# Kernel optimization log

Measured on AMD Instinct MI355X. Metric: run time of the kernel, lower is better.

The kernel has to match this reference:

```python
import jax, jax.numpy as jnp
import numpy as np

HEADS = 16
DIM = 1024


def setup_inputs() -> dict:
    key = jax.random.key(0)
    ks = jax.random.split(key, 9)
    b, n, d = 2, 2048, DIM
    scale = 1.0 / np.sqrt(d)  # xavier-ish scale for weights
    x = jax.random.normal(ks[0], (b, n, d), dtype=jnp.float32)
    Wq = jax.random.normal(ks[1], (d, d), dtype=jnp.float32) * scale
    Wk = jax.random.normal(ks[2], (d, d), dtype=jnp.float32) * scale
    Wv = jax.random.normal(ks[3], (d, d), dtype=jnp.float32) * scale
    Wo = jax.random.normal(ks[4], (d, d), dtype=jnp.float32) * scale
    bq = jnp.zeros((d,), jnp.float32)
    bk = jnp.zeros((d,), jnp.float32)
    bv = jnp.zeros((d,), jnp.float32)
    bo = jnp.zeros((d,), jnp.float32)
    return {"x": x, "Wq": Wq, "bq": bq, "Wk": Wk, "bk": bk,
            "Wv": Wv, "bv": bv, "Wo": Wo, "bo": bo}


def reference(x, Wq, bq, Wk, bk, Wv, bv, Wo, bo):
    b, n, d = x.shape
    h = HEADS
    hd = d // h
    # torch Linear: y = x @ W.T + b  (W stored [out, in]; here square so W given as [d,d])
    q = x @ Wq.T + bq
    k = x @ Wk.T + bk
    v = x @ Wv.T + bv
    # b n (h d) -> b h n d
    q = q.reshape(b, n, h, hd).transpose(0, 2, 1, 3)
    k = k.reshape(b, n, h, hd).transpose(0, 2, 1, 3)
    v = v.reshape(b, n, h, hd).transpose(0, 2, 1, 3)
    # NOTE: scale is 1/sqrt(dim), not 1/sqrt(head_dim), faithful to source.
    scores = jnp.einsum('bhqd,bhkd->bhqk', q, k) / jnp.sqrt(jnp.float32(d))
    attn = jax.nn.softmax(scores, axis=-1)
    out = jnp.einsum('bhqk,bhkd->bhqd', attn, v)
    out = out.transpose(0, 2, 1, 3).reshape(b, n, d)  # b h n d -> b n (h d)
    return out @ Wo.T + bo
```

## Files before the change

### kernel.cpp

```cpp
#include <hip/hip_runtime.h>

typedef unsigned short u16t;
typedef __attribute__((ext_vector_type(8))) short bf16x8;
typedef __attribute__((ext_vector_type(4))) float f32x4;

#define DM   1024
#define SEQL 2048
#define NHD  16
#define HDD  64

#define GLL16(g, l) __builtin_amdgcn_global_load_lds( \
    (const __attribute__((address_space(1))) void*)(g), \
    (__attribute__((address_space(3))) void*)(l), 16, 0, 0)

#if defined(__has_builtin)
#if __has_builtin(__builtin_amdgcn_exp2f)
#define EXP2(x) __builtin_amdgcn_exp2f(x)
#else
#define EXP2(x) exp2f(x)
#endif
#else
#define EXP2(x) exp2f(x)
#endif

__device__ __forceinline__ u16t f2bf(float f) {
  unsigned u = __float_as_uint(f);
  return (u16t)((u + 0x7fffu + ((u >> 16) & 1u)) >> 16);
}
__device__ __forceinline__ unsigned pack_bf16_2(float a, float b) {
  const unsigned ua = __float_as_uint(a) + 0x8000u;
  const unsigned ub = __float_as_uint(b) + 0x8000u;
  return __builtin_amdgcn_perm(ub, ua, 0x07060302);
}

struct ConvArgs { const float* src[5]; u16t* dst[5]; };

__global__ __launch_bounds__(256) void conv_kernel(ConvArgs a) {
  const int gid = blockIdx.x * 256 + threadIdx.x;
  const int e = gid << 2;
  int sel, off;
  if (e < 4194304) { sel = 0; off = e; }
  else { const int r = e - 4194304; sel = 1 + (r >> 20); off = r & 1048575; }
  const float4 f = *(const float4*)(a.src[sel] + off);
  union { u16t s[4]; uint2 u; } o;
  o.s[0] = f2bf(f.x); o.s[1] = f2bf(f.y); o.s[2] = f2bf(f.z); o.s[3] = f2bf(f.w);
  *(uint2*)(a.dst[sel] + off) = o.u;
}

__device__ __forceinline__ int gslot(int m, int kc) { return (m << 2) + (kc ^ ((m >> 1) & 3)); }

template<int MODE>
__device__ __forceinline__ void qkv_body(
    const u16t* __restrict__ X, const u16t* __restrict__ W,
    const float* __restrict__ bias, float oscale, u16t* __restrict__ outB,
    u16t* smem)
{
  u16t* const Es = smem;

  const int tid = threadIdx.x;
  const int l = tid & 63, w = tid >> 6, q = l >> 4, ln = l & 15;
  const int trow0 = blockIdx.y << 7;
  const int dcol0 = blockIdx.x << 7;
  const int wm = (w >> 1) << 6, wn = (w & 1) << 6;

  const int s0 = (w << 6) + l, s1 = s0 + 256;
  const int m0 = s0 >> 2, kc0 = (s0 & 3) ^ ((m0 >> 1) & 3);
  const int m1 = s1 >> 2, kc1 = (s1 & 3) ^ ((m1 >> 1) & 3);
  const u16t* gA0 = X + (size_t)(trow0 + m0) * DM + (kc0 << 3);
  const u16t* gA1 = X + (size_t)(trow0 + m1) * DM + (kc1 << 3);
  const u16t* gB0 = W + (size_t)(dcol0 + m0) * DM + (kc0 << 3);
  const u16t* gB1 = W + (size_t)(dcol0 + m1) * DM + (kc1 << 3);
  const int dO0 = (w << 6) << 3;
  const int dO1 = ((w << 6) + 256) << 3;

  f32x4 acc[4][4] = {};

  GLL16(gA0, smem + dO0);
  GLL16(gA1, smem + dO1);
  GLL16(gB0, smem + 4096 + dO0);
  GLL16(gB1, smem + 4096 + dO1);

  for (int kt = 0; kt < DM; kt += 32) {
    const int it = kt >> 5;
    u16t* const curA = smem + ((it & 1) ? 8192 : 0);
    u16t* const curB = curA + 4096;
    __syncthreads();
    if (kt + 32 < DM) {
      u16t* const nA = smem + ((it & 1) ? 0 : 8192);
      u16t* const nB = nA + 4096;
      GLL16(gA0 + kt + 32, nA + dO0);
      GLL16(gA1 + kt + 32, nA + dO1);
      GLL16(gB0 + kt + 32, nB + dO0);
      GLL16(gB1 + kt + 32, nB + dO1);
    }

    bf16x8 af[4], bfr[4];
    #pragma unroll
    for (int mi = 0; mi < 4; ++mi) {
      const int r = wm + (mi << 4) + ln;
      af[mi] = *(const bf16x8*)&((MODE == 1 ? curB : curA)[gslot(r, q) << 3]);
    }
    #pragma unroll
    for (int ni = 0; ni < 4; ++ni) {
      const int r = wn + (ni << 4) + ln;
      bfr[ni] = *(const bf16x8*)&((MODE == 1 ? curA : curB)[gslot(r, q) << 3]);
    }
    #pragma unroll
    for (int mi = 0; mi < 4; ++mi)
      #pragma unroll
      for (int ni = 0; ni < 4; ++ni)
        acc[mi][ni] = __builtin_amdgcn_mfma_f32_16x16x32_bf16(af[mi], bfr[ni], acc[mi][ni], 0, 0, 0);
  }

  __syncthreads();

  if (MODE == 1) {
    #pragma unroll
    for (int mi = 0; mi < 4; ++mi) {
      const int dl = wm + (mi << 4) + (q << 2);
      const float4 b4 = *(const float4*)&bias[dcol0 + dl];
      #pragma unroll
      for (int ni = 0; ni < 4; ++ni) {
        const int tl = wn + (ni << 4) + ln;
        uint2 pk;
        pk.x = pack_bf16_2((acc[mi][ni][0] + b4.x) * oscale, (acc[mi][ni][1] + b4.y) * oscale);
        pk.y = pack_bf16_2((acc[mi][ni][2] + b4.z) * oscale, (acc[mi][ni][3] + b4.w) * oscale);
        *(uint2*)&Es[tl * 136 + dl] = pk;
      }
    }
    __syncthreads();
    #pragma unroll
    for (int it = 0; it < 8; ++it) {
      const int u = (it << 8) + tid;
      const int tl = u >> 4, c8 = u & 15;
      const uint4 vv = *(const uint4*)&Es[tl * 136 + (c8 << 3)];
      const int tok = trow0 + tl;
      const int b = tok >> 11, n = tok & (SEQL - 1);
      const int dg = dcol0 + (c8 << 3);
      const int h = dg >> 6, hd = dg & 63;
      *(uint4*)&outB[((size_t)(b * NHD + h) * SEQL + n) * HDD + hd] = vv;
    }
  } else {
    #pragma unroll
    for (int ni = 0; ni < 4; ++ni) {
      const int dl = wn + (ni << 4) + ln;
      const float bv = bias[dcol0 + dl];
      #pragma unroll
      for (int mi = 0; mi < 4; ++mi) {
        const int g = (wm >> 2) + (mi << 2) + q;
        const int g6 = g & 15;
        const int gp = (g & 16) | (g6 & 8) | ((g6 & 3) << 1) | ((g6 >> 2) & 1);
        uint2 pk;
        pk.x = pack_bf16_2(acc[mi][ni][0] + bv, acc[mi][ni][1] + bv);
        pk.y = pack_bf16_2(acc[mi][ni][2] + bv, acc[mi][ni][3] + bv);
        *(uint2*)&Es[dl * 136 + (gp << 2)] = pk;
      }
    }
    __syncthreads();
    #pragma unroll
    for (int it = 0; it < 8; ++it) {
      const int u = (it << 8) + tid;
      const int dl = u >> 4, c8 = u & 15;
      const uint4 vv = *(const uint4*)&Es[dl * 136 + (c8 << 3)];
      const int dg = dcol0 + dl;
      const int h = dg >> 6, hd = dg & 63;
      const int b = trow0 >> 11;
      const int n = (trow0 & (SEQL - 1)) + (c8 << 3);
      *(uint4*)&outB[((size_t)(b * NHD + h) * HDD + hd) * SEQL + n] = vv;
    }
  }
}

struct QKVArgs { const u16t* W[3]; const float* b[3]; u16t* dst[3]; };

__global__ __launch_bounds__(256) void qkv_kernel(const u16t* __restrict__ X, QKVArgs g) {
  __shared__ alignas(16) u16t smem[17408];
  const int z = blockIdx.z;
  if (z == 2)      qkv_body<2>(X, g.W[2], g.b[2], 1.0f, g.dst[2], smem);
  else if (z == 1) qkv_body<1>(X, g.W[1], g.b[1], 1.0f, g.dst[1], smem);
  else             qkv_body<1>(X, g.W[0], g.b[0], 0.04508422f, g.dst[0], smem);
}

__global__ __launch_bounds__(256, 4) void attn_kernel(
    const u16t* __restrict__ Qb, const u16t* __restrict__ Kb,
    const u16t* __restrict__ Vt, u16t* __restrict__ ctx)
{
  __shared__ alignas(16) u16t smem[16384];

  const int tid = threadIdx.x;
  const int l = tid & 63, w = tid >> 6;
  const int q = l >> 4, ln = l & 15;
  const int bh = blockIdx.x, q0 = blockIdx.y << 7;
  const size_t hb = (size_t)bh * SEQL * HDD;
  const u16t* Qg = Qb + hb;
  const u16t* Kg = Kb + hb;
  const u16t* Vg = Vt + hb;

  bf16x8 qf[2][2];
  #pragma unroll
  for (int g = 0; g < 2; ++g) {
    const int qr = q0 + (w << 5) + (g << 4) + ln;
    #pragma unroll
    for (int ks = 0; ks < 2; ++ks)
      qf[g][ks] = *(const bf16x8*)(Qg + (size_t)qr * HDD + (((ks << 2) + q) << 3));
  }

  const int u0 = tid,       r0 = u0 >> 3, c0 = (u0 & 7) ^ (r0 & 7);
  const int u1 = 256 + tid, r1 = u1 >> 3, c1 = (u1 & 7) ^ (r1 & 7);
  const u16t* const kS0 = Kg + (size_t)r0 * HDD + (c0 << 3);
  const u16t* const kS1 = Kg + (size_t)r1 * HDD + (c1 << 3);
  const u16t* const vS0 = Vg + (size_t)r0 * SEQL + (c0 << 3);
  const u16t* const vS1 = Vg + (size_t)r1 * SEQL + (c1 << 3);
  const int dK0 = (w << 6) << 3, dK1 = (256 + (w << 6)) << 3;

  GLL16(kS0, smem + dK0);
  GLL16(kS1, smem + dK1);
  GLL16(vS0, smem + 4096 + dK0);
  GLL16(vS1, smem + 4096 + dK1);

  const short one_s = (short)0x3F80;
  const bf16x8 ones = { one_s, one_s, one_s, one_s, one_s, one_s, one_s, one_s };

  f32x4 accO[2][4] = {};
  f32x4 accL[2] = {};

  for (int t = 0; t < 32; ++t) {
    const int cb = (t & 1) ? 8192 : 0;
    u16t* const Ks = smem + cb;
    u16t* const Vs = smem + cb + 4096;
    __syncthreads();
    if (t + 1 < 32) {
      const int nb = (t & 1) ? 0 : 8192;
      const int ko = (t + 1) << 6;
      GLL16(kS0 + (size_t)ko * HDD, smem + nb + dK0);
      GLL16(kS1 + (size_t)ko * HDD, smem + nb + dK1);
      GLL16(vS0 + ko, smem + nb + 4096 + dK0);
      GLL16(vS1 + ko, smem + nb + 4096 + dK1);
    }

    f32x4 sc[2][4] = {{}, {}};
    __builtin_amdgcn_s_setprio(1);
    #pragma unroll
    for (int ks = 0; ks < 2; ++ks) {
      const int hc = (ks << 2) + q;
      #pragma unroll
      for (int ni = 0; ni < 4; ++ni) {
        const int kr = (ni << 4) + ln;
        const bf16x8 ak = *(const bf16x8*)&Ks[((kr << 3) + (hc ^ (kr & 7))) << 3];
        #pragma unroll
        for (int g = 0; g < 2; ++g)
          sc[g][ni] = __builtin_amdgcn_mfma_f32_16x16x32_bf16(ak, qf[g][ks], sc[g][ni], 0, 0, 0);
      }
    }
    __builtin_amdgcn_s_setprio(0);

    unsigned pk01[2][4], pk23[2][4];
    #pragma unroll
    for (int g = 0; g < 2; ++g)
      #pragma unroll
      for (int ni = 0; ni < 4; ++ni) {
        const float e0 = EXP2(sc[g][ni][0]);
        const float e1 = EXP2(sc[g][ni][1]);
        const float e2 = EXP2(sc[g][ni][2]);
        const float e3 = EXP2(sc[g][ni][3]);
        pk01[g][ni] = pack_bf16_2(e0, e1);
        pk23[g][ni] = pack_bf16_2(e2, e3);
      }

    __builtin_amdgcn_s_setprio(1);
    #pragma unroll
    for (int ks = 0; ks < 2; ++ks) {
      union { unsigned u[4]; bf16x8 v; } bfv[2];
      #pragma unroll
      for (int g = 0; g < 2; ++g) {
        bfv[g].u[0] = pk01[g][(ks << 1) + 0];
        bfv[g].u[1] = pk23[g][(ks << 1) + 0];
        bfv[g].u[2] = pk01[g][(ks << 1) + 1];
        bfv[g].u[3] = pk23[g][(ks << 1) + 1];
      }
      #pragma unroll
      for (int g = 0; g < 2; ++g)
        accL[g] = __builtin_amdgcn_mfma_f32_16x16x32_bf16(ones, bfv[g].v, accL[g], 0, 0, 0);
      const int c = (ks << 2) + q;
      #pragma unroll
      for (int nio = 0; nio < 4; ++nio) {
        const int vr = (nio << 4) + ln;
        const bf16x8 av = *(const bf16x8*)&Vs[((vr << 3) + (c ^ (vr & 7))) << 3];
        #pragma unroll
        for (int g = 0; g < 2; ++g)
          accO[g][nio] = __builtin_amdgcn_mfma_f32_16x16x32_bf16(av, bfv[g].v, accO[g][nio], 0, 0, 0);
      }
    }
    __builtin_amdgcn_s_setprio(0);
  }

  __syncthreads();
  #pragma unroll
  for (int g = 0; g < 2; ++g) {
    const float inv = 1.0f / accL[g][0];
    const int tl = (w << 5) + (g << 4) + ln;
    #pragma unroll
    for (int nio = 0; nio < 4; ++nio) {
      uint2 pk;
      pk.x = pack_bf16_2(accO[g][nio][0] * inv, accO[g][nio][1] * inv);
      pk.y = pack_bf16_2(accO[g][nio][2] * inv, accO[g][nio][3] * inv);
      *(uint2*)&smem[tl * 72 + (nio << 4) + (q << 2)] = pk;
    }
  }
  __syncthreads();
  const int h = bh & (NHD - 1), bi = bh >> 4;
  #pragma unroll
  for (int it = 0; it < 4; ++it) {
    const int u = (it << 8) + tid;
    const int tl = u >> 3, c8 = u & 7;
    const uint4 vv = *(const uint4*)&smem[tl * 72 + (c8 << 3)];
    *(uint4*)&ctx[((size_t)(bi * SEQL + q0 + tl)) * DM + (h << 6) + (c8 << 3)] = vv;
  }
}

__global__ __launch_bounds__(256) void outproj_kernel(
    const u16t* __restrict__ A, const u16t* __restrict__ W,
    const float* __restrict__ bias, float* __restrict__ outF)
{
  __shared__ alignas(16) u16t smem[24576];

  const int tid = threadIdx.x;
  const int l = tid & 63, w = tid >> 6, q = l >> 4, ln = l & 15;
  const int row0 = blockIdx.y << 7;
  const int col0 = blockIdx.x << 6;
  const int wm = (w >> 1) << 6, wn = (w & 1) << 5;

  const u16t* gA[4]; const u16t* gB[2];
  int dA[4], dB[2];
  #pragma unroll
  for (int p = 0; p < 4; ++p) {
    const int s = tid + (p << 8);
    const int m = s >> 3, kc = (s & 7) ^ (m & 7);
    gA[p] = A + (size_t)(row0 + m) * DM + (kc << 3);
    dA[p] = s << 3;
  }
  #pragma unroll
  for (int p = 0; p < 2; ++p) {
    const int s = tid + (p << 8);
    const int m = s >> 3, kc = (s & 7) ^ (m & 7);
    gB[p] = W + (size_t)(col0 + m) * DM + (kc << 3);
    dB[p] = s << 3;
  }

  f32x4 acc[4][2] = {};

  #pragma unroll
  for (int p = 0; p < 4; ++p) GLL16(gA[p], smem + dA[p]);
  #pragma unroll
  for (int p = 0; p < 2; ++p) GLL16(gB[p], smem + 8192 + dB[p]);

  for (int t = 0; t < 16; ++t) {
    u16t* const curA = smem + ((t & 1) ? 12288 : 0);
    u16t* const curB = smem + ((t & 1) ? 20480 : 8192);
    __syncthreads();
    if (t + 1 < 16) {
      u16t* const nA = smem + ((t & 1) ? 0 : 12288);
      u16t* const nB = smem + ((t & 1) ? 8192 : 20480);
      const int kt = (t + 1) << 6;
      #pragma unroll
      for (int p = 0; p < 4; ++p) GLL16(gA[p] + kt, nA + dA[p]);
      #pragma unroll
      for (int p = 0; p < 2; ++p) GLL16(gB[p] + kt, nB + dB[p]);
    }

    #pragma unroll
    for (int ks = 0; ks < 2; ++ks) {
      const int hc = (ks << 2) + q;
      bf16x8 af[4], bfr[2];
      #pragma unroll
      for (int mi = 0; mi < 4; ++mi) {
        const int r = wm + (mi << 4) + ln;
        af[mi] = *(const bf16x8*)&curA[((r << 3) + (hc ^ (r & 7))) << 3];
      }
      #pragma unroll
      for (int ni = 0; ni < 2; ++ni) {
        const int r = wn + (ni << 4) + ln;
        bfr[ni] = *(const bf16x8*)&curB[((r << 3) + (hc ^ (r & 7))) << 3];
      }
      #pragma unroll
      for (int mi = 0; mi < 4; ++mi)
        #pragma unroll
        for (int ni = 0; ni < 2; ++ni)
          acc[mi][ni] = __builtin_amdgcn_mfma_f32_16x16x32_bf16(af[mi], bfr[ni], acc[mi][ni], 0, 0, 0);
    }
  }

  #pragma unroll
  for (int ni = 0; ni < 2; ++ni) {
    const int col = col0 + wn + (ni << 4) + ln;
    const float bv = bias[col];
    #pragma unroll
    for (int mi = 0; mi < 4; ++mi)
      #pragma unroll
      for (int r = 0; r < 4; ++r) {
        const int row = row0 + wm + (mi << 4) + (q << 2) + r;
        outF[(size_t)row * DM + col] = acc[mi][ni][r] + bv;
      }
  }
}

extern "C" void kernel_launch(void* const* d_in, const int* in_sizes, int n_in,
                              void* d_out, int out_size, void* d_ws, size_t ws_size,
                              hipStream_t stream)
{
  const float* x  = (const float*)d_in[0];
  const float* Wq = (const float*)d_in[1];
  const float* bq = (const float*)d_in[2];
  const float* Wk = (const float*)d_in[3];
  const float* bk = (const float*)d_in[4];
  const float* Wv = (const float*)d_in[5];
  const float* bv = (const float*)d_in[6];
  const float* Wo = (const float*)d_in[7];
  const float* bo = (const float*)d_in[8];
  float* out = (float*)d_out;

  u16t* p = (u16t*)d_ws;
  u16t* xb  = p;  p += 4194304;
  u16t* Wqb = p;  p += 1048576;
  u16t* Wkb = p;  p += 1048576;
  u16t* Wvb = p;  p += 1048576;
  u16t* Wob = p;  p += 1048576;
  u16t* Qbf = p;  p += 4194304;
  u16t* Kbf = p;  p += 4194304;
  u16t* Vtb = p;  p += 4194304;
  u16t* ctx = p;  p += 4194304;

  ConvArgs ca;
  ca.src[0] = x;  ca.dst[0] = xb;
  ca.src[1] = Wq; ca.dst[1] = Wqb;
  ca.src[2] = Wk; ca.dst[2] = Wkb;
  ca.src[3] = Wv; ca.dst[3] = Wvb;
  ca.src[4] = Wo; ca.dst[4] = Wob;
  conv_kernel<<<8192, 256, 0, stream>>>(ca);

  QKVArgs qa;
  qa.W[0] = Wqb; qa.W[1] = Wkb; qa.W[2] = Wvb;
  qa.b[0] = bq;  qa.b[1] = bk;  qa.b[2] = bv;
  qa.dst[0] = Qbf; qa.dst[1] = Kbf; qa.dst[2] = Vtb;
  qkv_kernel<<<dim3(8, 32, 3), 256, 0, stream>>>(xb, qa);

  attn_kernel<<<dim3(32, 16), 256, 0, stream>>>(Qbf, Kbf, Vtb, ctx);

  outproj_kernel<<<dim3(16, 32), 256, 0, stream>>>(ctx, Wob, bo, out);
}
```

Before: 173.6 us.

## Fuse Q and K projections in one block sharing the X tile

Blocks with z=0 now compute both the Q and K projection tiles, loading each X tile into LDS once and reusing it for two weight tiles, so the grid drops from three to two z-slices. This removes redundant X loads and LDS staging for K. In exchange it doubles accumulator registers per thread, raises LDS use, and creates a load imbalance between the fused QK blocks and the V-only blocks.

```diff
diff --git a/kernel.cpp b/kernel.cpp
--- a/kernel.cpp
+++ b/kernel.cpp
@@ -49,11 +49,11 @@
 
 __device__ __forceinline__ int gslot(int m, int kc) { return (m << 2) + (kc ^ ((m >> 1) & 3)); }
 
-template<int MODE>
-__device__ __forceinline__ void qkv_body(
-    const u16t* __restrict__ X, const u16t* __restrict__ W,
-    const float* __restrict__ bias, float oscale, u16t* __restrict__ outB,
-    u16t* smem)
+__device__ __forceinline__ void qk_fused_body(
+    const u16t* __restrict__ X, const u16t* __restrict__ Wq,
+    const u16t* __restrict__ Wk, const float* __restrict__ bq,
+    const float* __restrict__ bk, u16t* __restrict__ Qo,
+    u16t* __restrict__ Ko, u16t* smem)
 {
   u16t* const Es = smem;
 
@@ -63,7 +63,117 @@
   const int dcol0 = blockIdx.x << 7;
   const int wm = (w >> 1) << 6, wn = (w & 1) << 6;
 
-  const int s0 = (w << 6) + l, s1 = s0 + 256;
+  const int s0 = tid, s1 = tid + 256;
+  const int m0 = s0 >> 2, kc0 = (s0 & 3) ^ ((m0 >> 1) & 3);
+  const int m1 = s1 >> 2, kc1 = (s1 & 3) ^ ((m1 >> 1) & 3);
+  const u16t* gX0 = X  + (size_t)(trow0 + m0) * DM + (kc0 << 3);
+  const u16t* gX1 = X  + (size_t)(trow0 + m1) * DM + (kc1 << 3);
+  const u16t* gQ0 = Wq + (size_t)(dcol0 + m0) * DM + (kc0 << 3);
+  const u16t* gQ1 = Wq + (size_t)(dcol0 + m1) * DM + (kc1 << 3);
+  const u16t* gK0 = Wk + (size_t)(dcol0 + m0) * DM + (kc0 << 3);
+  const u16t* gK1 = Wk + (size_t)(dcol0 + m1) * DM + (kc1 << 3);
+  const int dO0 = (w << 6) << 3;
+  const int dO1 = ((w << 6) + 256) << 3;
+
+  f32x4 accQ[4][4] = {};
+  f32x4 accK[4][4] = {};
+
+  GLL16(gX0, smem + dO0);
+  GLL16(gX1, smem + dO1);
+  GLL16(gQ0, smem + 4096 + dO0);
+  GLL16(gQ1, smem + 4096 + dO1);
+  GLL16(gK0, smem + 8192 + dO0);
+  GLL16(gK1, smem + 8192 + dO1);
+
+  for (int kt = 0; kt < DM; kt += 32) {
+    const int it = kt >> 5;
+    u16t* const curX  = smem + ((it & 1) ? 12288 : 0);
+    u16t* const curWq = curX + 4096;
+    u16t* const curWk = curX + 8192;
+    __syncthreads();
+    if (kt + 32 < DM) {
+      u16t* const nX = smem + ((it & 1) ? 0 : 12288);
+      GLL16(gX0 + kt + 32, nX + dO0);
+      GLL16(gX1 + kt + 32, nX + dO1);
+      GLL16(gQ0 + kt + 32, nX + 4096 + dO0);
+      GLL16(gQ1 + kt + 32, nX + 4096 + dO1);
+      GLL16(gK0 + kt + 32, nX + 8192 + dO0);
+      GLL16(gK1 + kt + 32, nX + 8192 + dO1);
+    }
+
+    bf16x8 bfr[4];
+    #pragma unroll
+    for (int ni = 0; ni < 4; ++ni)
+      bfr[ni] = *(const bf16x8*)&curX[gslot(wn + (ni << 4) + ln, q) << 3];
+
+    bf16x8 afQ[4], afK[4];
+    #pragma unroll
+    for (int mi = 0; mi < 4; ++mi) {
+      const int r = wm + (mi << 4) + ln;
+      afQ[mi] = *(const bf16x8*)&curWq[gslot(r, q) << 3];
+      afK[mi] = *(const bf16x8*)&curWk[gslot(r, q) << 3];
+    }
+    #pragma unroll
+    for (int mi = 0; mi < 4; ++mi)
+      #pragma unroll
+      for (int ni = 0; ni < 4; ++ni)
+        accQ[mi][ni] = __builtin_amdgcn_mfma_f32_16x16x32_bf16(afQ[mi], bfr[ni], accQ[mi][ni], 0, 0, 0);
+    #pragma unroll
+    for (int mi = 0; mi < 4; ++mi)
+      #pragma unroll
+      for (int ni = 0; ni < 4; ++ni)
+        accK[mi][ni] = __builtin_amdgcn_mfma_f32_16x16x32_bf16(afK[mi], bfr[ni], accK[mi][ni], 0, 0, 0);
+  }
+
+  #pragma unroll
+  for (int which = 0; which < 2; ++which) {
+    const float oscale = which ? 1.0f : 0.04508422f;
+    const float* const bias = which ? bk : bq;
+    u16t* const outB = which ? Ko : Qo;
+    __syncthreads();
+    #pragma unroll
+    for (int mi = 0; mi < 4; ++mi) {
+      const int dl = wm + (mi << 4) + (q << 2);
+      const float4 b4 = *(const float4*)&bias[dcol0 + dl];
+      #pragma unroll
+      for (int ni = 0; ni < 4; ++ni) {
+        const int tl = wn + (ni << 4) + ln;
+        const f32x4 a = which ? accK[mi][ni] : accQ[mi][ni];
+        uint2 pk;
+        pk.x = pack_bf16_2((a[0] + b4.x) * oscale, (a[1] + b4.y) * oscale);
+        pk.y = pack_bf16_2((a[2] + b4.z) * oscale, (a[3] + b4.w) * oscale);
+        *(uint2*)&Es[tl * 136 + dl] = pk;
+      }
+    }
+    __syncthreads();
+    #pragma unroll
+    for (int it = 0; it < 8; ++it) {
+      const int u = (it << 8) + tid;
+      const int tl = u >> 4, c8 = u & 15;
+      const uint4 vv = *(const uint4*)&Es[tl * 136 + (c8 << 3)];
+      const int tok = trow0 + tl;
+      const int b = tok >> 11, n = tok & (SEQL - 1);
+      const int dg = dcol0 + (c8 << 3);
+      const int h = dg >> 6, hd = dg & 63;
+      *(uint4*)&outB[((size_t)(b * NHD + h) * SEQL + n) * HDD + hd] = vv;
+    }
+  }
+}
+
+__device__ __forceinline__ void v_body(
+    const u16t* __restrict__ X, const u16t* __restrict__ W,
+    const float* __restrict__ bias, u16t* __restrict__ outB,
+    u16t* smem)
+{
+  u16t* const Es = smem;
+
+  const int tid = threadIdx.x;
+  const int l = tid & 63, w = tid >> 6, q = l >> 4, ln = l & 15;
+  const int trow0 = blockIdx.y << 7;
+  const int dcol0 = blockIdx.x << 7;
+  const int wm = (w >> 1) << 6, wn = (w & 1) << 6;
+
+  const int s0 = tid, s1 = tid + 256;
   const int m0 = s0 >> 2, kc0 = (s0 & 3) ^ ((m0 >> 1) & 3);
   const int m1 = s1 >> 2, kc1 = (s1 & 3) ^ ((m1 >> 1) & 3);
   const u16t* gA0 = X + (size_t)(trow0 + m0) * DM + (kc0 << 3);
@@ -96,15 +206,11 @@
 
     bf16x8 af[4], bfr[4];
     #pragma unroll
-    for (int mi = 0; mi < 4; ++mi) {
-      const int r = wm + (mi << 4) + ln;
-      af[mi] = *(const bf16x8*)&((MODE == 1 ? curB : curA)[gslot(r, q) << 3]);
-    }
-    #pragma unroll
-    for (int ni = 0; ni < 4; ++ni) {
-      const int r = wn + (ni << 4) + ln;
-      bfr[ni] = *(const bf16x8*)&((MODE == 1 ? curA : curB)[gslot(r, q) << 3]);
-    }
+    for (int mi = 0; mi < 4; ++mi)
+      af[mi] = *(const bf16x8*)&curA[gslot(wm + (mi << 4) + ln, q) << 3];
+    #pragma unroll
+    for (int ni = 0; ni < 4; ++ni)
+      bfr[ni] = *(const bf16x8*)&curB[gslot(wn + (ni << 4) + ln, q) << 3];
     #pragma unroll
     for (int mi = 0; mi < 4; ++mi)
       #pragma unroll
@@ -113,72 +219,43 @@
   }
 
   __syncthreads();
-
-  if (MODE == 1) {
+  #pragma unroll
+  for (int ni = 0; ni < 4; ++ni) {
+    const int dl = wn + (ni << 4) + ln;
+    const float bv = bias[dcol0 + dl];
     #pragma unroll
     for (int mi = 0; mi < 4; ++mi) {
-      const int dl = wm + (mi << 4) + (q << 2);
-      const float4 b4 = *(const float4*)&bias[dcol0 + dl];
-      #pragma unroll
-      for (int ni = 0; ni < 4; ++ni) {
-        const int tl = wn + (ni << 4) + ln;
-        uint2 pk;
-        pk.x = pack_bf16_2((acc[mi][ni][0] + b4.x) * oscale, (acc[mi][ni][1] + b4.y) * oscale);
-        pk.y = pack_bf16_2((acc[mi][ni][2] + b4.z) * oscale, (acc[mi][ni][3] + b4.w) * oscale);
-        *(uint2*)&Es[tl * 136 + dl] = pk;
-      }
-    }
-    __syncthreads();
-    #pragma unroll
-    for (int it = 0; it < 8; ++it) {
-      const int u = (it << 8) + tid;
-      const int tl = u >> 4, c8 = u & 15;
-      const uint4 vv = *(const uint4*)&Es[tl * 136 + (c8 << 3)];
-      const int tok = trow0 + tl;
-      const int b = tok >> 11, n = tok & (SEQL - 1);
-      const int dg = dcol0 + (c8 << 3);
-      const int h = dg >> 6, hd = dg & 63;
-      *(uint4*)&outB[((size_t)(b * NHD + h) * SEQL + n) * HDD + hd] = vv;
-    }
-  } else {
-    #pragma unroll
-    for (int ni = 0; ni < 4; ++ni) {
-      const int dl = wn + (ni << 4) + ln;
-      const float bv = bias[dcol0 + dl];
-      #pragma unroll
-      for (int mi = 0; mi < 4; ++mi) {
-        const int g = (wm >> 2) + (mi << 2) + q;
-        const int g6 = g & 15;
-        const int gp = (g & 16) | (g6 & 8) | ((g6 & 3) << 1) | ((g6 >> 2) & 1);
-        uint2 pk;
-        pk.x = pack_bf16_2(acc[mi][ni][0] + bv, acc[mi][ni][1] + bv);
-        pk.y = pack_bf16_2(acc[mi][ni][2] + bv, acc[mi][ni][3] + bv);
-        *(uint2*)&Es[dl * 136 + (gp << 2)] = pk;
-      }
-    }
-    __syncthreads();
-    #pragma unroll
-    for (int it = 0; it < 8; ++it) {
-      const int u = (it << 8) + tid;
-      const int dl = u >> 4, c8 = u & 15;
-      const uint4 vv = *(const uint4*)&Es[dl * 136 + (c8 << 3)];
-      const int dg = dcol0 + dl;
-      const int h = dg >> 6, hd = dg & 63;
-      const int b = trow0 >> 11;
-      const int n = (trow0 & (SEQL - 1)) + (c8 << 3);
-      *(uint4*)&outB[((size_t)(b * NHD + h) * HDD + hd) * SEQL + n] = vv;
-    }
+      const int g = (wm >> 2) + (mi << 2) + q;
+      const int g6 = g & 15;
+      const int gp = (g & 16) | (g6 & 8) | ((g6 & 3) << 1) | ((g6 >> 2) & 1);
+      uint2 pk;
+      pk.x = pack_bf16_2(acc[mi][ni][0] + bv, acc[mi][ni][1] + bv);
+      pk.y = pack_bf16_2(acc[mi][ni][2] + bv, acc[mi][ni][3] + bv);
+      *(uint2*)&Es[dl * 136 + (gp << 2)] = pk;
+    }
+  }
+  __syncthreads();
+  #pragma unroll
+  for (int it = 0; it < 8; ++it) {
+    const int u = (it << 8) + tid;
+    const int dl = u >> 4, c8 = u & 15;
+    const uint4 vv = *(const uint4*)&Es[dl * 136 + (c8 << 3)];
+    const int dg = dcol0 + dl;
+    const int h = dg >> 6, hd = dg & 63;
+    const int b = trow0 >> 11;
+    const int n = (trow0 & (SEQL - 1)) + (c8 << 3);
+    *(uint4*)&outB[((size_t)(b * NHD + h) * HDD + hd) * SEQL + n] = vv;
   }
 }
 
 struct QKVArgs { const u16t* W[3]; const float* b[3]; u16t* dst[3]; };
 
 __global__ __launch_bounds__(256) void qkv_kernel(const u16t* __restrict__ X, QKVArgs g) {
-  __shared__ alignas(16) u16t smem[17408];
-  const int z = blockIdx.z;
-  if (z == 2)      qkv_body<2>(X, g.W[2], g.b[2], 1.0f, g.dst[2], smem);
-  else if (z == 1) qkv_body<1>(X, g.W[1], g.b[1], 1.0f, g.dst[1], smem);
-  else             qkv_body<1>(X, g.W[0], g.b[0], 0.04508422f, g.dst[0], smem);
+  __shared__ alignas(16) u16t smem[24576];
+  if (blockIdx.z == 0)
+    qk_fused_body(X, g.W[0], g.W[1], g.b[0], g.b[1], g.dst[0], g.dst[1], smem);
+  else
+    v_body(X, g.W[2], g.b[2], g.dst[2], smem);
 }
 
 __global__ __launch_bounds__(256, 4) void attn_kernel(
@@ -442,7 +519,7 @@
   qa.W[0] = Wqb; qa.W[1] = Wkb; qa.W[2] = Wvb;
   qa.b[0] = bq;  qa.b[1] = bk;  qa.b[2] = bv;
   qa.dst[0] = Qbf; qa.dst[1] = Kbf; qa.dst[2] = Vtb;
-  qkv_kernel<<<dim3(8, 32, 3), 256, 0, stream>>>(xb, qa);
+  qkv_kernel<<<dim3(8, 32, 2), 256, 0, stream>>>(xb, qa);
 
   attn_kernel<<<dim3(32, 16), 256, 0, stream>>>(Qbf, Kbf, Vtb, ctx);
 
```

After: 185.8 us. +7.0%, slower.
